# Kernel tuning notes

Measured on AMD Instinct MI355X. Metric: run time of the kernel, lower is better.

## Reference

```python
import jax, jax.numpy as jnp
import numpy as np

# Model config (matches init_kwargs)
B, N, D = 4, 4096, 1024
H, DH = 16, 64            # heads, dim_head (H*DH == D)
SEG, RATIO = 64, 2        # LongNet segment length and dilation ratio
DFF = 4 * D
EPS = 1e-5


def layer_norm(x, g, b):
    m = jnp.mean(x, axis=-1, keepdims=True)
    v = jnp.var(x, axis=-1, keepdims=True)
    return (x - m) * jax.lax.rsqrt(v + EPS) * g + b


def dilated_attention(x, wq, bq, wk, bk, wv, bv, wo, bo):
    # LongNet-style dilated attention: split into segments of SEG tokens,
    # each head attends over every RATIO-th token of its segment, with the
    # dilation offset distributed across heads (offset = head % RATIO).
    b, n, d = x.shape
    G = n // SEG          # number of segments
    M = SEG // RATIO      # dilated segment length
    scale = DH ** -0.5

    def proj_split(w, bias):
        t = (x @ w + bias).reshape(b, G, SEG, H, DH)
        return t.transpose(0, 1, 3, 2, 4)  # [B, G, H, SEG, DH]

    q = proj_split(wq, bq)
    k = proj_split(wk, bk)
    v = proj_split(wv, bv)

    # per-head dilated indices within a segment: [H, M]
    idx = (jnp.arange(H)[:, None] % RATIO) + RATIO * jnp.arange(M)[None, :]
    gidx = idx[None, None, :, :, None]  # broadcast to [1,1,H,M,1]
    qs = jnp.take_along_axis(q, gidx, axis=3)  # [B,G,H,M,DH]
    ks = jnp.take_along_axis(k, gidx, axis=3)
    vs = jnp.take_along_axis(v, gidx, axis=3)

    scores = jnp.einsum('bghmd,bghnd->bghmn', qs, ks) * scale
    p = jax.nn.softmax(scores, axis=-1)
    o = jnp.einsum('bghmn,bghnd->bghmd', p, vs)  # [B,G,H,M,DH]

    # scatter dilated outputs back to full segment positions (zeros elsewhere)
    full = jnp.zeros((b, G, H, SEG, DH), dtype=o.dtype)
    full = full.at[:, :, jnp.arange(H)[:, None], idx, :].set(o)
    out = full.transpose(0, 1, 3, 2, 4).reshape(b, n, d)
    return out @ wo + bo


def setup_inputs() -> dict:
    key = jax.random.key(0)
    ks = jax.random.split(key, 8)
    sd = D ** -0.5
    inp = {
        'x': jax.random.normal(ks[0], (B, N, D), jnp.float32),
        'gamma': jnp.ones((D,), jnp.float32),  # shared pre-norm (beta is zero buffer)
        'wq': jax.random.normal(ks[1], (D, D), jnp.float32) * sd,
        'bq': jnp.zeros((D,), jnp.float32),
        'wk': jax.random.normal(ks[2], (D, D), jnp.float32) * sd,
        'bk': jnp.zeros((D,), jnp.float32),
        'wv': jax.random.normal(ks[3], (D, D), jnp.float32) * sd,
        'bv': jnp.zeros((D,), jnp.float32),
        'wo': jax.random.normal(ks[4], (D, D), jnp.float32) * sd,
        'bo': jnp.zeros((D,), jnp.float32),
        'ff_g': jnp.ones((D,), jnp.float32),   # FFN LayerNorm weight
        'ff_b': jnp.zeros((D,), jnp.float32),  # FFN LayerNorm bias
        'w1': jax.random.normal(ks[5], (D, DFF), jnp.float32) * sd,
        'b1': jnp.zeros((DFF,), jnp.float32),
        'w2': jax.random.normal(ks[6], (DFF, D), jnp.float32) * (DFF ** -0.5),
        'b2': jnp.zeros((D,), jnp.float32),
    }
    return inp


def reference(x, gamma, wq, bq, wk, bk, wv, bv, wo, bo, ff_g, ff_b, w1, b1, w2, b2):
    zero = jnp.zeros((D,), x.dtype)
    # attention sub-block (pre-norm, residual)
    h = layer_norm(x, gamma, zero)
    attn = dilated_attention(h, wq, bq, wk, bk, wv, bv, wo, bo)
    x = x + attn
    # FFN sub-block (outer shared norm, then FFN's own LayerNorm per FeedForward)
    h = layer_norm(x, gamma, zero)
    h = layer_norm(h, ff_g, ff_b)
    h = jax.nn.gelu(h @ w1 + b1, approximate=False) @ w2 + b2
    return x + h
```

## Files before the change

kernel.cpp:

```cpp
#include <hip/hip_runtime.h>
#include <hip/hip_bf16.h>
#include <math.h>

#define NTOK 16384
#define DM   1024
#define NQKV 3072
#define DFF  4096

typedef __bf16 bf16;
typedef __bf16 bf16x8 __attribute__((ext_vector_type(8)));
typedef float  f32x4  __attribute__((ext_vector_type(4)));

__device__ __forceinline__ void gload_lds16(const bf16* g, bf16* l) {
  __builtin_amdgcn_global_load_lds((const __attribute__((address_space(1))) void*)g,
                                   (__attribute__((address_space(3))) void*)l,
                                   16, 0, 0);
}

#define BAR()    asm volatile("s_barrier" ::: "memory")
#define SB0()    __builtin_amdgcn_sched_barrier(0)
#define LGKM0()  asm volatile("s_waitcnt lgkmcnt(0)" ::: "memory")
#define VMW(N)   asm volatile("s_waitcnt vmcnt(" #N ")" ::: "memory")

__device__ __forceinline__ float fast_gelu(float v) {
  const float u  = 0.79788456080286536f * (v + 0.044715f * v * v * v);
  const float e  = __expf(2.0f * u);
  const float th = 1.0f - 2.0f / (e + 1.0f);
  return 0.5f * v * (1.0f + th);
}

__device__ __forceinline__ void map_block(int nblk, int& row0, int& col0) {
  int id = blockIdx.x;
  id = (id & 7) * (nblk >> 3) + (id >> 3);
  const int ncol = nblk >> 7;
  const int gsz  = ncol << 3;
  const int grp  = id / gsz;
  const int rem  = id - grp * gsz;
  row0 = ((grp << 3) + (rem & 7)) << 7;
  col0 = (rem >> 3) << 7;
}

__device__ __forceinline__ size_t tile_off(int rowg, int k, int KB) {
  const int rr = rowg & 127;
  const int swz = (rr & 3) ^ ((rr >> 2) & 3);
  const int slot = ((k >> 3) & 3) ^ swz;
  return ((size_t)(rowg >> 7) * KB + (k >> 5)) * 4096 + rr * 32 + slot * 8 + (k & 7);
}

__global__ __launch_bounds__(256)
void transpose_cvt(const float* __restrict__ src, bf16* __restrict__ dst, int K, int N)
{
  __shared__ float t[32][33];
  const int tx = threadIdx.x & 31, ty = threadIdx.x >> 5;
  const int n0 = blockIdx.x * 32, k0 = blockIdx.y * 32;
#pragma unroll
  for (int i = 0; i < 4; ++i)
    t[ty + 8*i][tx] = src[(size_t)(k0 + ty + 8*i) * N + n0 + tx];
  __syncthreads();
#pragma unroll
  for (int i = 0; i < 4; ++i)
    dst[(size_t)(n0 + ty + 8*i) * K + k0 + tx] = (bf16)t[tx][ty + 8*i];
}

__global__ __launch_bounds__(256)
void transpose_cvt_tiled(const float* __restrict__ s0, const float* __restrict__ s1,
                         const float* __restrict__ s2, bf16* __restrict__ dst,
                         int K, int Nper)
{
  __shared__ float t[32][33];
  const int tx = threadIdx.x & 31, ty = threadIdx.x >> 5;
  const int n0 = blockIdx.x * 32, k0 = blockIdx.y * 32;
  const int z = blockIdx.z;
  const float* src = (z == 0) ? s0 : (z == 1) ? s1 : s2;
  const int KB = K >> 5;
#pragma unroll
  for (int i = 0; i < 4; ++i)
    t[ty + 8*i][tx] = src[(size_t)(k0 + ty + 8*i) * Nper + n0 + tx];
  __syncthreads();
#pragma unroll
  for (int i = 0; i < 4; ++i) {
    const int ng = z * Nper + n0 + ty + 8*i;
    dst[tile_off(ng, k0 + tx, KB)] = (bf16)t[tx][ty + 8*i];
  }
}

__global__ void concat_bias(const float* __restrict__ bq, const float* __restrict__ bk,
                            const float* __restrict__ bv, float* __restrict__ o)
{
  int i = blockIdx.x * 256 + threadIdx.x;
  o[i] = (i < 1024) ? bq[i] : (i < 2048 ? bk[i - 1024] : bv[i - 2048]);
}

__global__ __launch_bounds__(256)
void ln1_kernel(const float* __restrict__ x, const float* __restrict__ gamma,
                bf16* __restrict__ out)
{
  __shared__ float2 red[4];
  const int row = blockIdx.x, tid = threadIdx.x;
  const float4 v = ((const float4*)(x + (size_t)row * DM))[tid];
  float s  = v.x + v.y + v.z + v.w;
  float s2 = v.x*v.x + v.y*v.y + v.z*v.z + v.w*v.w;
#pragma unroll
  for (int m = 32; m >= 1; m >>= 1) { s += __shfl_xor(s, m); s2 += __shfl_xor(s2, m); }
  if ((tid & 63) == 0) red[tid >> 6] = make_float2(s, s2);
  __syncthreads();
  float S  = red[0].x + red[1].x + red[2].x + red[3].x;
  float S2 = red[0].y + red[1].y + red[2].y + red[3].y;
  const float mean = S * (1.0f / DM);
  const float var  = S2 * (1.0f / DM) - mean * mean;
  const float rs   = rsqrtf(var + 1e-5f);
  const float4 g = ((const float4*)gamma)[tid];
  union { bf16 b[4]; uint2 u; } o;
  o.b[0] = (bf16)((v.x - mean) * rs * g.x);
  o.b[1] = (bf16)((v.y - mean) * rs * g.y);
  o.b[2] = (bf16)((v.z - mean) * rs * g.z);
  o.b[3] = (bf16)((v.w - mean) * rs * g.w);
  *(uint2*)(out + tile_off(row, tid * 4, DM >> 5)) = o.u;
}

__global__ __launch_bounds__(256)
void ln2_kernel(const float* __restrict__ x, const float* __restrict__ gamma,
                const float* __restrict__ ffg, const float* __restrict__ ffb,
                bf16* __restrict__ out)
{
  __shared__ float2 red[4];
  const int row = blockIdx.x, tid = threadIdx.x;
  const float4 v = ((const float4*)(x + (size_t)row * DM))[tid];
  float s  = v.x + v.y + v.z + v.w;
  float s2 = v.x*v.x + v.y*v.y + v.z*v.z + v.w*v.w;
#pragma unroll
  for (int m = 32; m >= 1; m >>= 1) { s += __shfl_xor(s, m); s2 += __shfl_xor(s2, m); }
  if ((tid & 63) == 0) red[tid >> 6] = make_float2(s, s2);
  __syncthreads();
  float S  = red[0].x + red[1].x + red[2].x + red[3].x;
  float S2 = red[0].y + red[1].y + red[2].y + red[3].y;
  float mean = S * (1.0f / DM);
  float var  = S2 * (1.0f / DM) - mean * mean;
  float rs   = rsqrtf(var + 1e-5f);
  const float4 g = ((const float4*)ffg)[tid];
  const float4 gg = ((const float4*)gamma)[tid];
  float y0 = (v.x - mean) * rs * gg.x;
  float y1 = (v.y - mean) * rs * gg.y;
  float y2 = (v.z - mean) * rs * gg.z;
  float y3 = (v.w - mean) * rs * gg.w;
  __syncthreads();
  s  = y0 + y1 + y2 + y3;
  s2 = y0*y0 + y1*y1 + y2*y2 + y3*y3;
#pragma unroll
  for (int m = 32; m >= 1; m >>= 1) { s += __shfl_xor(s, m); s2 += __shfl_xor(s2, m); }
  if ((tid & 63) == 0) red[tid >> 6] = make_float2(s, s2);
  __syncthreads();
  S  = red[0].x + red[1].x + red[2].x + red[3].x;
  S2 = red[0].y + red[1].y + red[2].y + red[3].y;
  mean = S * (1.0f / DM);
  var  = S2 * (1.0f / DM) - mean * mean;
  rs   = rsqrtf(var + 1e-5f);
  const float4 bb = ((const float4*)ffb)[tid];
  union { bf16 b[4]; uint2 u; } o;
  o.b[0] = (bf16)((y0 - mean) * rs * g.x + bb.x);
  o.b[1] = (bf16)((y1 - mean) * rs * g.y + bb.y);
  o.b[2] = (bf16)((y2 - mean) * rs * g.z + bb.z);
  o.b[3] = (bf16)((y3 - mean) * rs * g.w + bb.w);
  *(uint2*)(out + tile_off(row, tid * 4, DM >> 5)) = o.u;
}

template<int EPI>
__global__ __launch_bounds__(256, 4)
void gemm64d(const bf16* __restrict__ A, int lda,
             const bf16* __restrict__ Bt,
             const float* __restrict__ bias,
             const float* res, int ldres,
             void* Cout, int ldc, int K, int nblk)
{
  __shared__ __align__(16) bf16 lds[16384];
  const int tid = threadIdx.x, lane = tid & 63, wave = tid >> 6;
  const int wm = wave >> 1, wn = wave & 1;
  const int l16 = lane & 15, lg = lane >> 4;

  int row0, col0;
  map_block(nblk, row0, col0);
  const int NT = K >> 6;

  const char* Ab = (const char*)A;
  const char* Bb = (const char*)Bt;
  unsigned oA[4], oB[4];
  {
    const int lr = tid >> 3;
    const int lc = tid & 7;
#pragma unroll
    for (int it = 0; it < 4; ++it) {
      const int r = it * 32 + lr;
      const int gc = ((lc ^ (r & 7)) << 3);
      oA[it] = (unsigned)(((row0 + r) * lda + gc) * 2);
      oB[it] = (unsigned)(((col0 + r) * K   + gc) * 2);
    }
  }

#define STAGE64() do { \
    gload_lds16((const bf16*)(Ab + oA[0]), lds         + tid * 8); \
    gload_lds16((const bf16*)(Ab + oA[1]), lds + 2048  + tid * 8); \
    gload_lds16((const bf16*)(Ab + oA[2]), lds + 4096  + tid * 8); \
    gload_lds16((const bf16*)(Ab + oA[3]), lds + 6144  + tid * 8); \
    gload_lds16((const bf16*)(Bb + oB[0]), lds + 8192  + tid * 8); \
    gload_lds16((const bf16*)(Bb + oB[1]), lds + 10240 + tid * 8); \
    gload_lds16((const bf16*)(Bb + oB[2]), lds + 12288 + tid * 8); \
    gload_lds16((const bf16*)(Bb + oB[3]), lds + 14336 + tid * 8); \
    oA[0] += 128; oA[1] += 128; oA[2] += 128; oA[3] += 128; \
    oB[0] += 128; oB[1] += 128; oB[2] += 128; oB[3] += 128; } while (0)

  int aoff[4][2], boff[4][2];
#pragma unroll
  for (int i = 0; i < 4; ++i) {
    const int ra = wm * 64 + i * 16 + l16;
    const int rb = wn * 64 + i * 16 + l16;
#pragma unroll
    for (int kk = 0; kk < 2; ++kk) {
      aoff[i][kk] = ra * 64 + (((kk * 4 + lg) ^ (ra & 7)) << 3);
      boff[i][kk] = 8192 + rb * 64 + (((kk * 4 + lg) ^ (rb & 7)) << 3);
    }
  }

  f32x4 acc[4][4] = {};

  STAGE64();
  VMW(0); BAR();
  for (int t = 0; t < NT; ++t) {
    bf16x8 af[4][2], bf0[4];
#pragma unroll
    for (int i = 0; i < 4; ++i) {
      af[i][0] = *(const bf16x8*)&lds[aoff[i][0]];
      af[i][1] = *(const bf16x8*)&lds[aoff[i][1]];
      bf0[i]   = *(const bf16x8*)&lds[boff[i][0]];
    }
#pragma unroll
    for (int j = 0; j < 4; ++j)
#pragma unroll
      for (int i = 0; i < 4; ++i)
        acc[i][j] = __builtin_amdgcn_mfma_f32_16x16x32_bf16(af[i][0], bf0[j], acc[i][j], 0, 0, 0);
    bf16x8 bf1[4];
#pragma unroll
    for (int j = 0; j < 4; ++j)
      bf1[j] = *(const bf16x8*)&lds[boff[j][1]];
    LGKM0(); SB0();
    BAR();
    if (t + 1 < NT) STAGE64();
#pragma unroll
    for (int j = 0; j < 4; ++j)
#pragma unroll
      for (int i = 0; i < 4; ++i)
        acc[i][j] = __builtin_amdgcn_mfma_f32_16x16x32_bf16(af[i][1], bf1[j], acc[i][j], 0, 0, 0);
    VMW(0); BAR();
  }

#pragma unroll
  for (int i = 0; i < 4; ++i) {
    const int m0 = row0 + wm * 64 + i * 16 + lg * 4;
#pragma unroll
    for (int j = 0; j < 4; ++j) {
      const int n = col0 + wn * 64 + j * 16 + l16;
      const float bv = bias[n];
#pragma unroll
      for (int r = 0; r < 4; ++r) {
        const long m = m0 + r;
        float v = acc[i][j][r] + bv;
        if constexpr (EPI == 0) {
          ((bf16*)Cout)[m * ldc + n] = (bf16)v;
        } else if constexpr (EPI == 1) {
          ((float*)Cout)[m * ldc + n] = v + res[m * ldres + n];
        } else {
          ((bf16*)Cout)[m * ldc + n] = (bf16)fast_gelu(v);
        }
      }
    }
  }
}

template<int EPI>
__global__ __launch_bounds__(256, 4)
void gemm32c(const bf16* __restrict__ A,
             const bf16* __restrict__ Bt,
             const float* __restrict__ bias,
             const float* res, int ldres,
             void* Cout, int ldc, int K, int nblk)
{
  __shared__ __align__(16) bf16 lds[16384];
  const int tid = threadIdx.x, lane = tid & 63, wave = tid >> 6;
  const int wm = wave >> 1, wn = wave & 1;
  const int l16 = lane & 15, lg = lane >> 4;

  int row0, col0;
  map_block(nblk, row0, col0);
  const int NT = K >> 5;
  const int KB = K >> 5;

  const char* Ab = (const char*)A;
  const char* Bb = (const char*)Bt;
  unsigned oA = (unsigned)(((size_t)(row0 >> 7) * KB) * 8192) + tid * 16;
  unsigned oB = (unsigned)(((size_t)(col0 >> 7) * KB) * 8192) + tid * 16;

#define STAGE32(BASE) do { \
    gload_lds16((const bf16*)(Ab + oA),        lds + (BASE)        + tid * 8); \
    gload_lds16((const bf16*)(Ab + oA + 4096), lds + (BASE) + 2048 + tid * 8); \
    gload_lds16((const bf16*)(Bb + oB),        lds + (BASE) + 4096 + tid * 8); \
    gload_lds16((const bf16*)(Bb + oB + 4096), lds + (BASE) + 6144 + tid * 8); \
    oA += 8192; oB += 8192; } while (0)

  int aoff[4], boff[4];
#pragma unroll
  for (int i = 0; i < 4; ++i) {
    const int ra = wm * 64 + i * 16 + l16;
    const int rb = wn * 64 + i * 16 + l16;
    aoff[i] = ra * 32 + ((lg ^ (ra & 3) ^ ((ra >> 2) & 3)) << 3);
    boff[i] = 4096 + rb * 32 + ((lg ^ (rb & 3) ^ ((rb >> 2) & 3)) << 3);
  }

  f32x4 acc[4][4] = {};

#define TILE32(BASE, TI) do { \
    bf16x8 af[4], bfr[4]; \
    _Pragma("unroll") \
    for (int i = 0; i < 4; ++i) { \
      af[i]  = *(const bf16x8*)&lds[(BASE) + aoff[i]]; \
      bfr[i] = *(const bf16x8*)&lds[(BASE) + boff[i]]; \
    } \
    _Pragma("unroll") \
    for (int j = 0; j < 4; ++j) \
      _Pragma("unroll") \
      for (int i = 0; i < 4; ++i) \
        acc[i][j] = __builtin_amdgcn_mfma_f32_16x16x32_bf16(af[i], bfr[j], acc[i][j], 0, 0, 0); \
    LGKM0(); SB0(); \
    BAR(); \
    if ((TI) + 2 < NT) { STAGE32(BASE); VMW(4); } \
    else { VMW(0); } \
    BAR(); } while (0)

  STAGE32(0);
  STAGE32(8192);
  VMW(4);
  BAR();

  for (int t = 0; t < NT; t += 2) {
    TILE32(0, t);
    TILE32(8192, t + 1);
  }

#pragma unroll
  for (int i = 0; i < 4; ++i) {
    const int m0 = row0 + wm * 64 + i * 16 + lg * 4;
#pragma unroll
    for (int j = 0; j < 4; ++j) {
      const int n = col0 + wn * 64 + j * 16 + l16;
      const float bv = bias[n];
#pragma unroll
      for (int r = 0; r < 4; ++r) {
        const long m = m0 + r;
        float v = acc[i][j][r] + bv;
        if constexpr (EPI == 0) {
          ((bf16*)Cout)[m * ldc + n] = (bf16)v;
        } else if constexpr (EPI == 1) {
          ((float*)Cout)[m * ldc + n] = v + res[m * ldres + n];
        } else {
          ((bf16*)Cout)[m * ldc + n] = (bf16)fast_gelu(v);
        }
      }
    }
  }
}

__global__ __launch_bounds__(256)
void attn_kernel(bf16* qkv)
{
  __shared__ bf16 PldsA[4 * 32 * 32];
  __shared__ bf16 vTA[4 * 64 * 32];
  const int wave = threadIdx.x >> 6;
  const int lane = threadIdx.x & 63;
  bf16* Plds = PldsA + wave * 1024;
  bf16* vT   = vTA   + wave * 2048;
  const int blk = blockIdx.x * 4 + wave;
  const int h = blk & 15;
  const int g = (blk >> 4) & 63;
  const int b = blk >> 10;
  const int par = h & 1;
  const int l16 = lane & 15, lg = lane >> 4;
  const long base = ((long)b * 4096 + g * 64) * NQKV;

  bf16x8 qf[2][2], kf[2][2];
#pragma unroll
  for (int mb = 0; mb < 2; ++mb) {
    const int s = par + 2 * (mb * 16 + l16);
    const bf16* qrow = qkv + base + (long)s * NQKV + h * 64;
#pragma unroll
    for (int kk = 0; kk < 2; ++kk) {
      qf[mb][kk] = *(const bf16x8*)(qrow + kk * 32 + lg * 8);
      kf[mb][kk] = *(const bf16x8*)(qrow + 1024 + kk * 32 + lg * 8);
    }
  }

#pragma unroll
  for (int it = 0; it < 4; ++it) {
    const int kr  = it * 8 + (lane >> 3);
    const int dh0 = (lane & 7) * 8;
    const int s = par + 2 * kr;
    union { uint4 u; bf16 e[8]; } vv;
    vv.u = *(const uint4*)(qkv + base + (long)s * NQKV + 2048 + h * 64 + dh0);
#pragma unroll
    for (int j = 0; j < 8; ++j)
      vT[(dh0 + j) * 32 + kr] = vv.e[j];
  }

  f32x4 sc[2][2] = {};
#pragma unroll
  for (int mb = 0; mb < 2; ++mb)
#pragma unroll
    for (int nb = 0; nb < 2; ++nb)
#pragma unroll
      for (int kk = 0; kk < 2; ++kk)
        sc[mb][nb] = __builtin_amdgcn_mfma_f32_16x16x32_bf16(qf[mb][kk], kf[nb][kk], sc[mb][nb], 0, 0, 0);

  float pr[2][2][4];
#pragma unroll
  for (int mb = 0; mb < 2; ++mb)
#pragma unroll
    for (int r = 0; r < 4; ++r) {
      float a0 = sc[mb][0][r] * 0.125f, a1 = sc[mb][1][r] * 0.125f;
      float mx = fmaxf(a0, a1);
#pragma unroll
      for (int msk = 8; msk >= 1; msk >>= 1) mx = fmaxf(mx, __shfl_xor(mx, msk));
      float e0 = expf(a0 - mx), e1 = expf(a1 - mx);
      float sm = e0 + e1;
#pragma unroll
      for (int msk = 8; msk >= 1; msk >>= 1) sm += __shfl_xor(sm, msk);
      float inv = 1.0f / sm;
      pr[mb][0][r] = e0 * inv;
      pr[mb][1][r] = e1 * inv;
    }

  __syncthreads();
#pragma unroll
  for (int mb = 0; mb < 2; ++mb)
#pragma unroll
    for (int nb = 0; nb < 2; ++nb)
#pragma unroll
      for (int r = 0; r < 4; ++r)
        Plds[(mb * 16 + lg * 4 + r) * 32 + nb * 16 + l16] = (bf16)pr[mb][nb][r];
  __syncthreads();

  bf16x8 pa[2], vb[4];
#pragma unroll
  for (int mb = 0; mb < 2; ++mb)
    pa[mb] = *(const bf16x8*)&Plds[(mb * 16 + l16) * 32 + lg * 8];
#pragma unroll
  for (int nb = 0; nb < 4; ++nb)
    vb[nb] = *(const bf16x8*)&vT[(nb * 16 + l16) * 32 + lg * 8];
  f32x4 oc[2][4] = {};
#pragma unroll
  for (int mb = 0; mb < 2; ++mb)
#pragma unroll
    for (int nb = 0; nb < 4; ++nb)
      oc[mb][nb] = __builtin_amdgcn_mfma_f32_16x16x32_bf16(pa[mb], vb[nb], oc[mb][nb], 0, 0, 0);

#pragma unroll
  for (int mb = 0; mb < 2; ++mb)
#pragma unroll
    for (int nb = 0; nb < 4; ++nb)
#pragma unroll
      for (int r = 0; r < 4; ++r) {
        const int m = mb * 16 + lg * 4 + r;
        const int s = par + 2 * m;
        qkv[base + (long)s * NQKV + h * 64 + nb * 16 + l16] = (bf16)oc[mb][nb][r];
      }
  const uint4 z = make_uint4(0, 0, 0, 0);
#pragma unroll
  for (int it = 0; it < 4; ++it) {
    const int r2 = it * 8 + (lane >> 3);
    const int s = (1 - par) + 2 * r2;
    *(uint4*)(qkv + base + (long)s * NQKV + h * 64 + (lane & 7) * 8) = z;
  }
}

extern "C" void kernel_launch(void* const* d_in, const int* in_sizes, int n_in,
                              void* d_out, int out_size, void* d_ws, size_t ws_size,
                              hipStream_t stream)
{
  const float* x     = (const float*)d_in[0];
  const float* gamma = (const float*)d_in[1];
  const float* wq = (const float*)d_in[2];  const float* bq = (const float*)d_in[3];
  const float* wk = (const float*)d_in[4];  const float* bk = (const float*)d_in[5];
  const float* wv = (const float*)d_in[6];  const float* bv = (const float*)d_in[7];
  const float* wo = (const float*)d_in[8];  const float* bo = (const float*)d_in[9];
  const float* ffg = (const float*)d_in[10]; const float* ffb = (const float*)d_in[11];
  const float* w1 = (const float*)d_in[12]; const float* b1 = (const float*)d_in[13];
  const float* w2 = (const float*)d_in[14]; const float* b2 = (const float*)d_in[15];

  char* p = (char*)d_ws;
  bf16* Wqkv_t = (bf16*)p; p += (size_t)NQKV * DM * 2;
  bf16* Wo_t   = (bf16*)p; p += (size_t)DM * DM * 2;
  bf16* W1_t   = (bf16*)p; p += (size_t)DFF * DM * 2;
  bf16* W2_t   = (bf16*)p; p += (size_t)DM * DFF * 2;
  float* bqkv  = (float*)p; p += (size_t)NQKV * 4;
  bf16* hbuf   = (bf16*)p; p += (size_t)NTOK * DM * 2;
  bf16* qkv    = (bf16*)p; p += (size_t)NTOK * DFF * 2;
  float* xnew  = (float*)d_out;

  dim3 b256(256);
  transpose_cvt_tiled<<<dim3(32, 32, 3),  b256, 0, stream>>>(wq, wk, wv, Wqkv_t, DM, DM);
  transpose_cvt      <<<dim3(32, 32),     b256, 0, stream>>>(wo, Wo_t, DM, DM);
  transpose_cvt_tiled<<<dim3(128, 32, 1), b256, 0, stream>>>(w1, w1, w1, W1_t, DM, DFF);
  transpose_cvt      <<<dim3(32, 128),    b256, 0, stream>>>(w2, W2_t, DFF, DM);
  concat_bias<<<12, b256, 0, stream>>>(bq, bk, bv, bqkv);

  ln1_kernel<<<NTOK, b256, 0, stream>>>(x, gamma, hbuf);

  gemm32c<0><<<dim3(128 * 24), b256, 0, stream>>>(
      hbuf, Wqkv_t, bqkv, nullptr, 0, qkv, NQKV, DM, 128 * 24);

  attn_kernel<<<1024, b256, 0, stream>>>(qkv);

  gemm64d<1><<<dim3(128 * 8), b256, 0, stream>>>(
      qkv, NQKV, Wo_t, bo, x, DM, xnew, DM, DM, 128 * 8);

  ln2_kernel<<<NTOK, b256, 0, stream>>>(xnew, gamma, ffg, ffb, hbuf);

  gemm32c<2><<<dim3(128 * 32), b256, 0, stream>>>(
      hbuf, W1_t, b1, nullptr, 0, qkv, DFF, DM, 128 * 32);

  gemm64d<1><<<dim3(128 * 8), b256, 0, stream>>>(
      qkv, DFF, W2_t, b2, xnew, DM, (float*)d_out, DM, DFF, 128 * 8);
}
```

Baseline: 552.9 us.

## Load B operand directly into registers in gemm32c, stage only A in LDS

In the gemm32c kernel, the B tiles are no longer staged through shared memory. Each wave loads its B fragments from global memory straight into registers, using precomputed swizzled offsets and a double register buffer. Only A still goes through LDS, so the shared allocation is halved and half the LDS reads per tile go away. In exchange it uses more VGPRs, waits on all outstanding memory ops (vmcnt(0)) every tile, and makes each wave issue its own B global loads, which may lose coalescing and prefetch depth.

```diff
diff --git a/kernel.cpp b/kernel.cpp
--- a/kernel.cpp
+++ b/kernel.cpp
@@ -283,7 +283,7 @@
              const float* res, int ldres,
              void* Cout, int ldc, int K, int nblk)
 {
-  __shared__ __align__(16) bf16 lds[16384];
+  __shared__ __align__(16) bf16 lds[8192];
   const int tid = threadIdx.x, lane = tid & 63, wave = tid >> 6;
   const int wm = wave >> 1, wn = wave & 1;
   const int l16 = lane & 15, lg = lane >> 4;
@@ -296,52 +296,65 @@
   const char* Ab = (const char*)A;
   const char* Bb = (const char*)Bt;
   unsigned oA = (unsigned)(((size_t)(row0 >> 7) * KB) * 8192) + tid * 16;
-  unsigned oB = (unsigned)(((size_t)(col0 >> 7) * KB) * 8192) + tid * 16;
-
-#define STAGE32(BASE) do { \
+
+  unsigned oBg0, oBg1, oBg2, oBg3;
+  {
+    const unsigned cb = (unsigned)(((size_t)(col0 >> 7) * KB) * 8192);
+    const int rb0 = wn * 64 + 0 * 16 + l16;
+    const int rb1 = wn * 64 + 1 * 16 + l16;
+    const int rb2 = wn * 64 + 2 * 16 + l16;
+    const int rb3 = wn * 64 + 3 * 16 + l16;
+    oBg0 = cb + 2 * (rb0 * 32 + ((lg ^ (rb0 & 3) ^ ((rb0 >> 2) & 3)) << 3));
+    oBg1 = cb + 2 * (rb1 * 32 + ((lg ^ (rb1 & 3) ^ ((rb1 >> 2) & 3)) << 3));
+    oBg2 = cb + 2 * (rb2 * 32 + ((lg ^ (rb2 & 3) ^ ((rb2 >> 2) & 3)) << 3));
+    oBg3 = cb + 2 * (rb3 * 32 + ((lg ^ (rb3 & 3) ^ ((rb3 >> 2) & 3)) << 3));
+  }
+
+#define STAGEA(BASE) do { \
     gload_lds16((const bf16*)(Ab + oA),        lds + (BASE)        + tid * 8); \
     gload_lds16((const bf16*)(Ab + oA + 4096), lds + (BASE) + 2048 + tid * 8); \
-    gload_lds16((const bf16*)(Bb + oB),        lds + (BASE) + 4096 + tid * 8); \
-    gload_lds16((const bf16*)(Bb + oB + 4096), lds + (BASE) + 6144 + tid * 8); \
-    oA += 8192; oB += 8192; } while (0)
-
-  int aoff[4], boff[4];
+    oA += 8192; } while (0)
+#define LOADB(dst) do { \
+    dst[0] = *(const bf16x8*)(Bb + oBg0); \
+    dst[1] = *(const bf16x8*)(Bb + oBg1); \
+    dst[2] = *(const bf16x8*)(Bb + oBg2); \
+    dst[3] = *(const bf16x8*)(Bb + oBg3); \
+    oBg0 += 8192; oBg1 += 8192; oBg2 += 8192; oBg3 += 8192; } while (0)
+
+  int aoff[4];
 #pragma unroll
   for (int i = 0; i < 4; ++i) {
     const int ra = wm * 64 + i * 16 + l16;
-    const int rb = wn * 64 + i * 16 + l16;
     aoff[i] = ra * 32 + ((lg ^ (ra & 3) ^ ((ra >> 2) & 3)) << 3);
-    boff[i] = 4096 + rb * 32 + ((lg ^ (rb & 3) ^ ((rb >> 2) & 3)) << 3);
   }
 
   f32x4 acc[4][4] = {};
-
-#define TILE32(BASE, TI) do { \
-    bf16x8 af[4], bfr[4]; \
+  bf16x8 bqA[4], bqB[4];
+
+#define TILE32(BASE, CUR, TI) do { \
+    bf16x8 af[4]; \
     _Pragma("unroll") \
-    for (int i = 0; i < 4; ++i) { \
-      af[i]  = *(const bf16x8*)&lds[(BASE) + aoff[i]]; \
-      bfr[i] = *(const bf16x8*)&lds[(BASE) + boff[i]]; \
-    } \
+    for (int i = 0; i < 4; ++i) \
+      af[i] = *(const bf16x8*)&lds[(BASE) + aoff[i]]; \
+    LGKM0(); SB0(); \
     _Pragma("unroll") \
     for (int j = 0; j < 4; ++j) \
       _Pragma("unroll") \
       for (int i = 0; i < 4; ++i) \
-        acc[i][j] = __builtin_amdgcn_mfma_f32_16x16x32_bf16(af[i], bfr[j], acc[i][j], 0, 0, 0); \
-    LGKM0(); SB0(); \
+        acc[i][j] = __builtin_amdgcn_mfma_f32_16x16x32_bf16(af[i], CUR[j], acc[i][j], 0, 0, 0); \
     BAR(); \
-    if ((TI) + 2 < NT) { STAGE32(BASE); VMW(4); } \
-    else { VMW(0); } \
+    VMW(0); \
+    if ((TI) + 2 < NT) { STAGEA(BASE); LOADB(CUR); } \
     BAR(); } while (0)
 
-  STAGE32(0);
-  STAGE32(8192);
-  VMW(4);
+  STAGEA(0);    LOADB(bqA);
+  VMW(0);
+  STAGEA(4096); LOADB(bqB);
   BAR();
 
   for (int t = 0; t < NT; t += 2) {
-    TILE32(0, t);
-    TILE32(8192, t + 1);
+    TILE32(0,    bqA, t);
+    TILE32(4096, bqB, t + 1);
   }
 
 #pragma unroll
```

Result: slower. 594.0 us (+7.4%).
